# Performance work log

Hardware: AMD Instinct MI355X
Metric: run time of the kernel (lower is better)

Reference implementation:

```python
import math
import jax, jax.numpy as jnp
import numpy as np

H = 16       # num_heads
DH = 128     # head_dim (q/k)
DV = 128     # value_head_dim
CHUNK = 1024 # chunk_size
BASE = 10000.0  # rope base


def _rope(q, k, start_index):
    # q, k: (B, L, H, Dh); rotate pair-split halves (x1|x2 layout, not interleaved)
    B, L, h, d = q.shape
    half = d // 2
    freqs = jnp.exp(jnp.arange(half, dtype=jnp.float32) * (-math.log(BASE) / half))
    t = (jnp.arange(L, dtype=jnp.float32) + start_index)[:, None] * freqs[None, :]  # (L, half)
    cos = jnp.cos(t)[None, :, None, :].astype(q.dtype)
    sin = jnp.sin(t)[None, :, None, :].astype(q.dtype)

    def rot(x):
        x1, x2 = jnp.split(x, 2, axis=-1)
        return jnp.concatenate([x1 * cos - x2 * sin, x2 * cos + x1 * sin], axis=-1)

    return rot(q), rot(k)


def setup_inputs() -> dict:
    key = jax.random.key(0)
    kq, kk, kv = jax.random.split(key, 3)
    B, L = 2, 4096
    q = jax.random.normal(kq, (B, L, H, DH), dtype=jnp.float32)
    k = jax.random.normal(kk, (B, L, H, DH), dtype=jnp.float32)
    v = jax.random.normal(kv, (B, L, H, DV), dtype=jnp.float32)
    return {"q": q, "k": k, "v": v, "start_index": 0}


def reference(q, k, v, start_index):
    # Training path of ChunkedSelfAttention: L > chunk_size, no cache/attn_mask.
    B, L, h, d = q.shape
    q, k = _rope(q, k, start_index)
    nc = L // CHUNK
    # (B, nc, H, C, D) -- chunks never attend across boundaries
    qc = q.reshape(B, nc, CHUNK, h, d).transpose(0, 1, 3, 2, 4)
    kc = k.reshape(B, nc, CHUNK, h, d).transpose(0, 1, 3, 2, 4)
    vc = v.reshape(B, nc, CHUNK, h, DV).transpose(0, 1, 3, 2, 4)
    scores = jnp.einsum('bnhqd,bnhkd->bnhqk', qc, kc) / math.sqrt(d)
    i = jnp.arange(CHUNK)
    causal = i[:, None] >= i[None, :]  # (C, C)
    scores = jnp.where(causal, scores, -jnp.inf)
    attn = jax.nn.softmax(scores.astype(jnp.float32), axis=-1).astype(q.dtype)
    out = jnp.einsum('bnhqk,bnhkv->bnhqv', attn, vc)
    out = out.transpose(0, 1, 3, 2, 4).reshape(B, L, h * DV)
    return out
```

## Files before the change

kernel.cpp:

```cpp
#include <hip/hip_runtime.h>
#include <math.h>

#define NB 2
#define SEQL 4096
#define NH 16
#define HD 128
#define HDV 128
#define CHK 1024
#define NC 4
#define BQ 128
#define BK 64
#define KSTR 136
#define VSTR 72
#define OUTW 2048
#define NEGB (-1e30f)
#define L2B64 0.20762050593045702f

typedef _Float16 f16x8 __attribute__((ext_vector_type(8)));
typedef float f32x4 __attribute__((ext_vector_type(4)));
typedef unsigned short u16x8 __attribute__((ext_vector_type(8)));

static __device__ __forceinline__ unsigned short f2h(float f) {
  return __builtin_bit_cast(unsigned short, (_Float16)f);
}
static __device__ __forceinline__ f16x8 ld8(const unsigned short* p) {
  return __builtin_bit_cast(f16x8, *(const u16x8*)p);
}
static __device__ __forceinline__ void fast_sincos(float t, float* sn, float* cs) {
  const float INV2PI = 0.15915494309189535f;
  const float TWOPI  = 6.283185307179586f;
  float rev = t * INV2PI;
  rev -= floorf(rev);
  float ang = rev * TWOPI;
  *sn = __sinf(ang);
  *cs = __cosf(ang);
}
static __device__ __forceinline__ void gload16(const void* g, void* l) {
  __builtin_amdgcn_global_load_lds(
      (const __attribute__((address_space(1))) unsigned int*)g,
      (__attribute__((address_space(3))) unsigned int*)l, 16, 0, 0);
}

#define DPPF(x, ctrl)                                                            \
  __builtin_bit_cast(float, __builtin_amdgcn_update_dpp(                         \
      __builtin_bit_cast(int, x), __builtin_bit_cast(int, x), ctrl, 0xF, 0xF, true))
static __device__ __forceinline__ float dpp16_max(float x) {
  x = fmaxf(x, DPPF(x, 0xB1));
  x = fmaxf(x, DPPF(x, 0x4E));
  x = fmaxf(x, DPPF(x, 0x141));
  x = fmaxf(x, DPPF(x, 0x140));
  return x;
}
static __device__ __forceinline__ float dpp16_sum(float x) {
  x += DPPF(x, 0xB1);
  x += DPPF(x, 0x4E);
  x += DPPF(x, 0x141);
  x += DPPF(x, 0x140);
  return x;
}

__global__ __launch_bounds__(256) void megalodon_prep(
    const float* __restrict__ k, const float* __restrict__ v,
    unsigned short* __restrict__ kr, unsigned short* __restrict__ vt,
    const int* __restrict__ startp) {
  const int tid = threadIdx.x;
  const int blk = blockIdx.x;
  if (blk < 4096) {
    const int s0 = startp[0];
    const int gr = blk * 32 + (tid >> 3);
    const int c0 = (tid & 7) * 8;
    const int h  = gr & 15;
    const int bl = gr >> 4;
    const int l  = bl & (SEQL - 1);
    const int b  = bl >> 12;
    const int n  = l >> 10;
    const int rc = l & (CHK - 1);
    const int jt = rc >> 6;
    const int r  = rc & 63;
    const float* kp = k + (size_t)gr * HD;
    float xa[8], xb[8];
    *(f32x4*)&xa[0] = *(const f32x4*)(kp + c0);
    *(f32x4*)&xa[4] = *(const f32x4*)(kp + c0 + 4);
    *(f32x4*)&xb[0] = *(const f32x4*)(kp + c0 + 64);
    *(f32x4*)&xb[4] = *(const f32x4*)(kp + c0 + 68);
    u16x8 lo, hi;
#pragma unroll
    for (int jj = 0; jj < 8; ++jj) {
      const int dd = c0 + jj;
      float freq = exp2f(-L2B64 * (float)dd);
      float t = (float)(l + s0) * freq;
      float sn, cs;
      fast_sincos(t, &sn, &cs);
      lo[jj] = f2h(xa[jj] * cs - xb[jj] * sn);
      hi[jj] = f2h(xb[jj] * cs + xa[jj] * sn);
    }
    unsigned short* dst = kr + ((size_t)(((b * NH + h) * NC + n) * 16 + jt)) * 8192;
    const int sw = (r & 7) << 3;
    *(u16x8*)&dst[(r * 128 + c0) ^ sw]      = lo;
    *(u16x8*)&dst[(r * 128 + c0 + 64) ^ sw] = hi;
  } else {
    const int tv = blk - 4096;
    const int jt = tv & 15;
    const int n  = (tv >> 4) & 3;
    const int h  = (tv >> 6) & 15;
    const int b  = tv >> 10;
    unsigned short* dst = vt + ((size_t)(((b * NH + h) * NC + n) * 16 + jt)) * 8192;
#pragma unroll
    for (int it = 0; it < 4; ++it) {
      const int idx = tid + it * 256;
      const int vc = idx & 127;
      const int kg = idx >> 7;
      const int lbase = n * CHK + jt * 64 + kg * 8;
      u16x8 vv;
#pragma unroll
      for (int i = 0; i < 8; ++i)
        vv[i] = f2h(v[((size_t)(b * SEQL + lbase + i) * NH + h) * HDV + vc]);
      *(u16x8*)&dst[(vc * 64 + kg * 8) ^ ((vc & 7) << 3)] = vv;
    }
  }
}

__global__ __launch_bounds__(256) void megalodon_attn2(
    const float* __restrict__ q,
    const unsigned short* __restrict__ kr,
    const unsigned short* __restrict__ vt,
    float* __restrict__ out,
    const int* __restrict__ startp) {

  __shared__ __align__(16) unsigned short smem[24576];

  const int tid  = threadIdx.x;
  const int lane = tid & 63;
  const int wv   = tid >> 6;
  const int ln15 = lane & 15;
  const int quad = lane >> 4;

  const int bid = blockIdx.x;
  const int qt = 7 - (bid >> 7);
  const int h  = bid & 15;
  const int n  = (bid >> 4) & 3;
  const int b  = (bid >> 6) & 1;

  const int s0 = startp[0];
  const float scale = 0.08838834764831845f;
  const int l0 = n * CHK + qt * BQ;

  f16x8 qf[2][4];
#pragma unroll
  for (int rt = 0; rt < 2; ++rt) {
    const int l = l0 + wv * 32 + rt * 16 + ln15;
    const float* qp = q + ((size_t)(b * SEQL + l) * NH + h) * HD;
#pragma unroll
    for (int kf2 = 0; kf2 < 2; ++kf2) {
      const int c0 = kf2 * 32 + quad * 8;
      float xa[8], xb[8];
      *(f32x4*)&xa[0] = *(const f32x4*)(qp + c0);
      *(f32x4*)&xa[4] = *(const f32x4*)(qp + c0 + 4);
      *(f32x4*)&xb[0] = *(const f32x4*)(qp + c0 + 64);
      *(f32x4*)&xb[4] = *(const f32x4*)(qp + c0 + 68);
      f16x8 lo, hi;
#pragma unroll
      for (int j = 0; j < 8; ++j) {
        const int dd = c0 + j;
        float x1 = xa[j];
        float x2 = xb[j];
        float freq = exp2f(-L2B64 * (float)dd);
        float t = (float)(l + s0) * freq;
        float sn, cs;
        fast_sincos(t, &sn, &cs);
        lo[j] = (_Float16)((x1 * cs - x2 * sn) * scale);
        hi[j] = (_Float16)((x2 * cs + x1 * sn) * scale);
      }
      qf[rt][kf2]     = lo;
      qf[rt][kf2 + 2] = hi;
    }
  }

  f32x4 oacc[2][8];
  float m_run[2][4], l_run[2][4];
#pragma unroll
  for (int rt = 0; rt < 2; ++rt) {
#pragma unroll
    for (int vq = 0; vq < 8; ++vq) { f32x4 z = {0.f, 0.f, 0.f, 0.f}; oacc[rt][vq] = z; }
#pragma unroll
    for (int rg = 0; rg < 4; ++rg) { m_run[rt][rg] = NEGB; l_run[rt][rg] = 0.f; }
  }

  const size_t tb0 = (size_t)(((b * NH + h) * NC + n)) * 16;
  const int ksw = (ln15 & 7) << 3;

  auto stageK = [&](int t) {
    const char* ks = (const char*)kr + ((tb0 + t) << 14) + wv * 4096 + lane * 16;
    char* kd = ((char*)smem) + ((t & 1) << 14) + wv * 4096;
#pragma unroll
    for (int i = 0; i < 4; ++i) gload16(ks + i * 1024, kd + i * 1024);
  };
  auto stageV = [&](int t) {
    const char* vs = (const char*)vt + ((tb0 + t) << 14) + wv * 4096 + lane * 16;
    char* vd = ((char*)smem) + 32768 + wv * 4096;
#pragma unroll
    for (int i = 0; i < 4; ++i) gload16(vs + i * 1024, vd + i * 1024);
  };

  const int ntiles = 2 * qt + 2;
  stageK(0);
  stageV(0);
  for (int j = 0; j < ntiles; ++j) {
    const int cur = j & 1;
    if (j + 1 < ntiles) {
      stageK(j + 1);
      asm volatile("s_waitcnt vmcnt(8)" ::: "memory");
    } else {
      asm volatile("s_waitcnt vmcnt(4)" ::: "memory");
    }
    __builtin_amdgcn_s_barrier();

    const unsigned short* sK  = smem + cur * 8192;
    const unsigned short* sVT = smem + 16384;
    const bool act = (j * BK <= qt * BQ + wv * 32 + 31);

    f32x4 sacc[2][4];
    if (act) {
#pragma unroll
      for (int rt = 0; rt < 2; ++rt)
#pragma unroll
        for (int ct = 0; ct < 4; ++ct) { f32x4 z = {0.f, 0.f, 0.f, 0.f}; sacc[rt][ct] = z; }
      __builtin_amdgcn_s_setprio(1);
#pragma unroll
      for (int ct = 0; ct < 4; ++ct) {
#pragma unroll
        for (int kf = 0; kf < 4; ++kf) {
          f16x8 kb = ld8(&sK[(((ct * 16 + ln15) * 128) + kf * 32 + quad * 8) ^ ksw]);
          sacc[0][ct] = __builtin_amdgcn_mfma_f32_16x16x32_f16(qf[0][kf], kb, sacc[0][ct], 0, 0, 0);
          sacc[1][ct] = __builtin_amdgcn_mfma_f32_16x16x32_f16(qf[1][kf], kb, sacc[1][ct], 0, 0, 0);
        }
      }
      __builtin_amdgcn_s_setprio(0);
    }

    __builtin_amdgcn_s_barrier();
    unsigned short* sP = smem + cur * 8192;

    if (act) {
      const int colb = j * BK + ln15;
      float alpha[2][4];
#pragma unroll
      for (int rt = 0; rt < 2; ++rt) {
        const int rowq = qt * BQ + wv * 32 + rt * 16 + quad * 4;
#pragma unroll
        for (int rg = 0; rg < 4; ++rg) {
          const int row = rowq + rg;
          float mx = NEGB;
#pragma unroll
          for (int ct = 0; ct < 4; ++ct) {
            float sv = sacc[rt][ct][rg];
            sv = (colb + ct * 16 <= row) ? sv : NEGB;
            sacc[rt][ct][rg] = sv;
            mx = fmaxf(mx, sv);
          }
          mx = dpp16_max(mx);
          float mo = m_run[rt][rg];
          float mn = fmaxf(mo, mx);
          m_run[rt][rg] = mn;
          float al = __expf(mo - mn);
          alpha[rt][rg] = al;
          float rs = 0.f;
          const int prow = rt * 16 + quad * 4 + rg;
          const int psw = ((quad * 4 + rg) & 7) << 3;
#pragma unroll
          for (int ct = 0; ct < 4; ++ct) {
            float p = __expf(sacc[rt][ct][rg] - mn);
            rs += p;
            sP[wv * 2048 + ((prow * 64 + ct * 16 + ln15) ^ psw)] = f2h(p);
          }
          rs = dpp16_sum(rs);
          l_run[rt][rg] = l_run[rt][rg] * al + rs;
        }
      }
#pragma unroll
      for (int rt = 0; rt < 2; ++rt)
#pragma unroll
        for (int vq = 0; vq < 8; ++vq)
#pragma unroll
          for (int rg = 0; rg < 4; ++rg) oacc[rt][vq][rg] *= alpha[rt][rg];
    }

    if (j + 1 < ntiles)
      asm volatile("s_waitcnt vmcnt(4)" ::: "memory");
    else
      asm volatile("s_waitcnt vmcnt(0)" ::: "memory");
    __builtin_amdgcn_s_barrier();

    if (act) {
      asm volatile("s_waitcnt lgkmcnt(0)" ::: "memory");
      __builtin_amdgcn_s_setprio(1);
#pragma unroll
      for (int kf = 0; kf < 2; ++kf) {
        f16x8 pa0 = ld8(&sP[wv * 2048 + ((ln15 * 64 + kf * 32 + quad * 8) ^ ksw)]);
        f16x8 pa1 = ld8(&sP[wv * 2048 + (((16 + ln15) * 64 + kf * 32 + quad * 8) ^ ksw)]);
#pragma unroll
        for (int vq = 0; vq < 8; ++vq) {
          f16x8 vb = ld8(&sVT[(((vq * 16 + ln15) * 64) + kf * 32 + quad * 8) ^ ksw]);
          oacc[0][vq] = __builtin_amdgcn_mfma_f32_16x16x32_f16(pa0, vb, oacc[0][vq], 0, 0, 0);
          oacc[1][vq] = __builtin_amdgcn_mfma_f32_16x16x32_f16(pa1, vb, oacc[1][vq], 0, 0, 0);
        }
      }
      __builtin_amdgcn_s_setprio(0);
    }

    __builtin_amdgcn_s_barrier();
    if (j + 1 < ntiles) stageV(j + 1);
  }

#pragma unroll
  for (int rt = 0; rt < 2; ++rt) {
#pragma unroll
    for (int rg = 0; rg < 4; ++rg) {
      const int l = l0 + wv * 32 + rt * 16 + quad * 4 + rg;
      const float lr = l_run[rt][rg];
      const float inv = (lr > 0.f) ? (1.0f / lr) : 0.f;
      float* op = out + (size_t)(b * SEQL + l) * OUTW + h * HDV + ln15;
#pragma unroll
      for (int vq = 0; vq < 8; ++vq)
        op[vq * 16] = oacc[rt][vq][rg] * inv;
    }
  }
}

__global__ __launch_bounds__(256) void megalodon_attn_k(
    const float* __restrict__ q,
    const float* __restrict__ k,
    const float* __restrict__ v,
    float* __restrict__ out,
    const int* __restrict__ startp) {

  __shared__ __align__(16) unsigned short smem[27136];
  unsigned short* sK  = smem;
  unsigned short* sVT = smem + 8704;
  unsigned short* sP  = smem + 17920;

  const int tid  = threadIdx.x;
  const int lane = tid & 63;
  const int wv   = tid >> 6;
  const int ln15 = lane & 15;
  const int quad = lane >> 4;

  const int bid = blockIdx.x;
  const int qt  = bid & 7;
  const int h   = (bid >> 3) & 15;
  const int n   = (bid >> 7) & 3;
  const int b   = bid >> 9;

  const int s0 = startp[0];
  const float scale = 0.08838834764831845f;
  const int l0 = n * CHK + qt * BQ;

  f16x8 qf[2][4];
#pragma unroll
  for (int rt = 0; rt < 2; ++rt) {
    const int l = l0 + wv * 32 + rt * 16 + ln15;
    const float* qp = q + ((size_t)(b * SEQL + l) * NH + h) * HD;
#pragma unroll
    for (int kf2 = 0; kf2 < 2; ++kf2) {
      const int c0 = kf2 * 32 + quad * 8;
      float xa[8], xb[8];
      *(f32x4*)&xa[0] = *(const f32x4*)(qp + c0);
      *(f32x4*)&xa[4] = *(const f32x4*)(qp + c0 + 4);
      *(f32x4*)&xb[0] = *(const f32x4*)(qp + c0 + 64);
      *(f32x4*)&xb[4] = *(const f32x4*)(qp + c0 + 68);
      f16x8 lo, hi;
#pragma unroll
      for (int j = 0; j < 8; ++j) {
        const int dd = c0 + j;
        float x1 = xa[j];
        float x2 = xb[j];
        float freq = exp2f(-L2B64 * (float)dd);
        float t = (float)(l + s0) * freq;
        float sn, cs;
        fast_sincos(t, &sn, &cs);
        lo[j] = (_Float16)((x1 * cs - x2 * sn) * scale);
        hi[j] = (_Float16)((x2 * cs + x1 * sn) * scale);
      }
      qf[rt][kf2]     = lo;
      qf[rt][kf2 + 2] = hi;
    }
  }

  f32x4 oacc[2][8];
  float m_run[2][4], l_run[2][4];
#pragma unroll
  for (int rt = 0; rt < 2; ++rt) {
#pragma unroll
    for (int vt = 0; vt < 8; ++vt) { f32x4 z = {0.f, 0.f, 0.f, 0.f}; oacc[rt][vt] = z; }
#pragma unroll
    for (int rg = 0; rg < 4; ++rg) { m_run[rt][rg] = NEGB; l_run[rt][rg] = 0.f; }
  }

  const float kfreq = exp2f(-L2B64 * (float)(tid & 63));

  const int ntiles = 2 * qt + 2;
  for (int j = 0; j < ntiles; ++j) {
    __syncthreads();
    const int kl0 = n * CHK + j * BK;

    for (int idx = tid; idx < BK * 64; idx += 256) {
      int r = idx >> 6, dd = idx & 63;
      int l = kl0 + r;
      const float* kp = k + ((size_t)(b * SEQL + l) * NH + h) * HD;
      float x1 = kp[dd];
      float x2 = kp[dd + 64];
      float t = (float)(l + s0) * kfreq;
      float sn, cs;
      fast_sincos(t, &sn, &cs);
      sK[r * KSTR + dd]      = f2h(x1 * cs - x2 * sn);
      sK[r * KSTR + dd + 64] = f2h(x2 * cs + x1 * sn);
    }
    for (int idx = tid; idx < HDV * (BK / 8); idx += 256) {
      int vc = idx & 127;
      int sk = idx >> 7;
      u16x8 vv;
#pragma unroll
      for (int i = 0; i < 8; ++i)
        vv[i] = f2h(v[((size_t)(b * SEQL + kl0 + sk * 8 + i) * NH + h) * HDV + vc]);
      *(u16x8*)&sVT[vc * VSTR + sk * 8] = vv;
    }
    __syncthreads();

    if (j * BK <= qt * BQ + wv * 32 + 31) {
      f32x4 sacc[2][4];
#pragma unroll
      for (int rt = 0; rt < 2; ++rt)
#pragma unroll
        for (int ct = 0; ct < 4; ++ct) { f32x4 z = {0.f, 0.f, 0.f, 0.f}; sacc[rt][ct] = z; }
#pragma unroll
      for (int ct = 0; ct < 4; ++ct) {
#pragma unroll
        for (int kf = 0; kf < 4; ++kf) {
          f16x8 kb = ld8(&sK[(ct * 16 + ln15) * KSTR + kf * 32 + quad * 8]);
          sacc[0][ct] = __builtin_amdgcn_mfma_f32_16x16x32_f16(qf[0][kf], kb, sacc[0][ct], 0, 0, 0);
          sacc[1][ct] = __builtin_amdgcn_mfma_f32_16x16x32_f16(qf[1][kf], kb, sacc[1][ct], 0, 0, 0);
        }
      }

      const int colb = j * BK + ln15;
      float alpha[2][4];
#pragma unroll
      for (int rt = 0; rt < 2; ++rt) {
        const int rowq = qt * BQ + wv * 32 + rt * 16 + quad * 4;
#pragma unroll
        for (int rg = 0; rg < 4; ++rg) {
          const int row = rowq + rg;
          float mx = NEGB;
#pragma unroll
          for (int ct = 0; ct < 4; ++ct) {
            float sv = sacc[rt][ct][rg];
            sv = (colb + ct * 16 <= row) ? sv : NEGB;
            sacc[rt][ct][rg] = sv;
            mx = fmaxf(mx, sv);
          }
          mx = fmaxf(mx, __shfl_xor(mx, 1));
          mx = fmaxf(mx, __shfl_xor(mx, 2));
          mx = fmaxf(mx, __shfl_xor(mx, 4));
          mx = fmaxf(mx, __shfl_xor(mx, 8));
          float mo = m_run[rt][rg];
          float mn = fmaxf(mo, mx);
          m_run[rt][rg] = mn;
          float al = __expf(mo - mn);
          alpha[rt][rg] = al;
          float rs = 0.f;
#pragma unroll
          for (int ct = 0; ct < 4; ++ct) {
            float p = __expf(sacc[rt][ct][rg] - mn);
            rs += p;
            sP[wv * (32 * VSTR) + (rt * 16 + quad * 4 + rg) * VSTR + ct * 16 + ln15] = f2h(p);
          }
          rs += __shfl_xor(rs, 1);
          rs += __shfl_xor(rs, 2);
          rs += __shfl_xor(rs, 4);
          rs += __shfl_xor(rs, 8);
          l_run[rt][rg] = l_run[rt][rg] * al + rs;
        }
      }
#pragma unroll
      for (int rt = 0; rt < 2; ++rt)
#pragma unroll
        for (int vt = 0; vt < 8; ++vt)
#pragma unroll
          for (int rg = 0; rg < 4; ++rg) oacc[rt][vt][rg] *= alpha[rt][rg];

      asm volatile("s_waitcnt lgkmcnt(0)" ::: "memory");

#pragma unroll
      for (int kf = 0; kf < 2; ++kf) {
        f16x8 pa0 = ld8(&sP[wv * (32 * VSTR) + (ln15)*VSTR + kf * 32 + quad * 8]);
        f16x8 pa1 = ld8(&sP[wv * (32 * VSTR) + (16 + ln15) * VSTR + kf * 32 + quad * 8]);
#pragma unroll
        for (int vt = 0; vt < 8; ++vt) {
          f16x8 vb = ld8(&sVT[(vt * 16 + ln15) * VSTR + kf * 32 + quad * 8]);
          oacc[0][vt] = __builtin_amdgcn_mfma_f32_16x16x32_f16(pa0, vb, oacc[0][vt], 0, 0, 0);
          oacc[1][vt] = __builtin_amdgcn_mfma_f32_16x16x32_f16(pa1, vb, oacc[1][vt], 0, 0, 0);
        }
      }
    }
  }

#pragma unroll
  for (int rt = 0; rt < 2; ++rt) {
#pragma unroll
    for (int rg = 0; rg < 4; ++rg) {
      const int l = l0 + wv * 32 + rt * 16 + quad * 4 + rg;
      const float lr = l_run[rt][rg];
      const float inv = (lr > 0.f) ? (1.0f / lr) : 0.f;
      float* op = out + (size_t)(b * SEQL + l) * OUTW + h * HDV + ln15;
#pragma unroll
      for (int vt = 0; vt < 8; ++vt)
        op[vt * 16] = oacc[rt][vt][rg] * inv;
    }
  }
}

extern "C" void kernel_launch(void* const* d_in, const int* in_sizes, int n_in,
                              void* d_out, int out_size, void* d_ws, size_t ws_size,
                              hipStream_t stream) {
  const float* q = (const float*)d_in[0];
  const float* k = (const float*)d_in[1];
  const float* v = (const float*)d_in[2];
  const int* start = (const int*)d_in[3];
  (void)in_sizes; (void)n_in; (void)out_size;

  const size_t NEED = 64ull * 1024 * 1024;
  if (d_ws != nullptr && ws_size >= NEED) {
    unsigned short* kr = (unsigned short*)d_ws;
    unsigned short* vt = kr + 16777216;
    megalodon_prep<<<6144, 256, 0, stream>>>(k, v, kr, vt, start);
    megalodon_attn2<<<NB * 4 * NH * 8, 256, 0, stream>>>(q, kr, vt, (float*)d_out, start);
  } else {
    megalodon_attn_k<<<NB * 4 * NH * 8, 256, 0, stream>>>(q, k, v, (float*)d_out, start);
  }
}
```

Measured before the change: 334.8 us.

## Use 8 waves of 16 rows each and double-buffer K and V together

The attention kernel moves from 4 waves with 32 query rows each to 8 waves with 16 rows each. This halves the per-wave registers for Q fragments, accumulators and softmax state, and launch bounds now request more resident waves. K and V tiles are loaded together into double-buffered shared memory, which removes a barrier and the separate V stage at the end of each iteration. Shared memory grows to 64KB, which can cap blocks per CU, and each K/V fragment read from LDS now feeds only one MFMA instead of two, so LDS traffic per FLOP doubles.

```diff
diff --git a/kernel.cpp b/kernel.cpp
--- a/kernel.cpp
+++ b/kernel.cpp
@@ -120,14 +120,14 @@
   }
 }
 
-__global__ __launch_bounds__(256) void megalodon_attn2(
+__global__ __launch_bounds__(512, 4) void megalodon_attn2(
     const float* __restrict__ q,
     const unsigned short* __restrict__ kr,
     const unsigned short* __restrict__ vt,
     float* __restrict__ out,
     const int* __restrict__ startp) {
 
-  __shared__ __align__(16) unsigned short smem[24576];
+  __shared__ __align__(16) unsigned short smem[32768];
 
   const int tid  = threadIdx.x;
   const int lane = tid & 63;
@@ -144,11 +144,11 @@
   const int s0 = startp[0];
   const float scale = 0.08838834764831845f;
   const int l0 = n * CHK + qt * BQ;
-
-  f16x8 qf[2][4];
-#pragma unroll
-  for (int rt = 0; rt < 2; ++rt) {
-    const int l = l0 + wv * 32 + rt * 16 + ln15;
+  const int rowbase = qt * BQ + wv * 16;
+
+  f16x8 qf[4];
+  {
+    const int l = l0 + wv * 16 + ln15;
     const float* qp = q + ((size_t)(b * SEQL + l) * NH + h) * HD;
 #pragma unroll
     for (int kf2 = 0; kf2 < 2; ++kf2) {
@@ -171,159 +171,127 @@
         lo[j] = (_Float16)((x1 * cs - x2 * sn) * scale);
         hi[j] = (_Float16)((x2 * cs + x1 * sn) * scale);
       }
-      qf[rt][kf2]     = lo;
-      qf[rt][kf2 + 2] = hi;
-    }
-  }
-
-  f32x4 oacc[2][8];
-  float m_run[2][4], l_run[2][4];
-#pragma unroll
-  for (int rt = 0; rt < 2; ++rt) {
-#pragma unroll
-    for (int vq = 0; vq < 8; ++vq) { f32x4 z = {0.f, 0.f, 0.f, 0.f}; oacc[rt][vq] = z; }
-#pragma unroll
-    for (int rg = 0; rg < 4; ++rg) { m_run[rt][rg] = NEGB; l_run[rt][rg] = 0.f; }
-  }
+      qf[kf2]     = lo;
+      qf[kf2 + 2] = hi;
+    }
+  }
+
+  f32x4 oacc[8];
+  float m_run[4], l_run[4];
+#pragma unroll
+  for (int vq = 0; vq < 8; ++vq) { f32x4 z = {0.f, 0.f, 0.f, 0.f}; oacc[vq] = z; }
+#pragma unroll
+  for (int rg = 0; rg < 4; ++rg) { m_run[rg] = NEGB; l_run[rg] = 0.f; }
 
   const size_t tb0 = (size_t)(((b * NH + h) * NC + n)) * 16;
   const int ksw = (ln15 & 7) << 3;
 
-  auto stageK = [&](int t) {
-    const char* ks = (const char*)kr + ((tb0 + t) << 14) + wv * 4096 + lane * 16;
-    char* kd = ((char*)smem) + ((t & 1) << 14) + wv * 4096;
-#pragma unroll
-    for (int i = 0; i < 4; ++i) gload16(ks + i * 1024, kd + i * 1024);
+  auto stage = [&](int t) {
+    const char* ks = (const char*)kr + ((tb0 + t) << 14) + wv * 2048 + lane * 16;
+    const char* vs = (const char*)vt + ((tb0 + t) << 14) + wv * 2048 + lane * 16;
+    char* kd = ((char*)smem) + ((t & 1) << 14) + wv * 2048;
+    char* vd = ((char*)smem) + 32768 + ((t & 1) << 14) + wv * 2048;
+    gload16(ks, kd);
+    gload16(ks + 1024, kd + 1024);
+    gload16(vs, vd);
+    gload16(vs + 1024, vd + 1024);
   };
-  auto stageV = [&](int t) {
-    const char* vs = (const char*)vt + ((tb0 + t) << 14) + wv * 4096 + lane * 16;
-    char* vd = ((char*)smem) + 32768 + wv * 4096;
-#pragma unroll
-    for (int i = 0; i < 4; ++i) gload16(vs + i * 1024, vd + i * 1024);
-  };
 
   const int ntiles = 2 * qt + 2;
-  stageK(0);
-  stageV(0);
+  stage(0);
   for (int j = 0; j < ntiles; ++j) {
     const int cur = j & 1;
     if (j + 1 < ntiles) {
-      stageK(j + 1);
-      asm volatile("s_waitcnt vmcnt(8)" ::: "memory");
+      stage(j + 1);
+      asm volatile("s_waitcnt vmcnt(4)" ::: "memory");
     } else {
-      asm volatile("s_waitcnt vmcnt(4)" ::: "memory");
+      asm volatile("s_waitcnt vmcnt(0)" ::: "memory");
     }
     __builtin_amdgcn_s_barrier();
 
     const unsigned short* sK  = smem + cur * 8192;
-    const unsigned short* sVT = smem + 16384;
-    const bool act = (j * BK <= qt * BQ + wv * 32 + 31);
-
-    f32x4 sacc[2][4];
+    const unsigned short* sVT = smem + 16384 + cur * 8192;
+    const bool act = (j * BK <= rowbase + 15);
+
+    f32x4 sacc[4];
     if (act) {
 #pragma unroll
-      for (int rt = 0; rt < 2; ++rt)
-#pragma unroll
-        for (int ct = 0; ct < 4; ++ct) { f32x4 z = {0.f, 0.f, 0.f, 0.f}; sacc[rt][ct] = z; }
+      for (int ct = 0; ct < 4; ++ct) { f32x4 z = {0.f, 0.f, 0.f, 0.f}; sacc[ct] = z; }
       __builtin_amdgcn_s_setprio(1);
 #pragma unroll
       for (int ct = 0; ct < 4; ++ct) {
 #pragma unroll
         for (int kf = 0; kf < 4; ++kf) {
           f16x8 kb = ld8(&sK[(((ct * 16 + ln15) * 128) + kf * 32 + quad * 8) ^ ksw]);
-          sacc[0][ct] = __builtin_amdgcn_mfma_f32_16x16x32_f16(qf[0][kf], kb, sacc[0][ct], 0, 0, 0);
-          sacc[1][ct] = __builtin_amdgcn_mfma_f32_16x16x32_f16(qf[1][kf], kb, sacc[1][ct], 0, 0, 0);
+          sacc[ct] = __builtin_amdgcn_mfma_f32_16x16x32_f16(qf[kf], kb, sacc[ct], 0, 0, 0);
         }
       }
       __builtin_amdgcn_s_setprio(0);
     }
 
     __builtin_amdgcn_s_barrier();
-    unsigned short* sP = smem + cur * 8192;
+    unsigned short* sP = smem + cur * 8192 + wv * 1024;
 
     if (act) {
       const int colb = j * BK + ln15;
-      float alpha[2][4];
-#pragma unroll
-      for (int rt = 0; rt < 2; ++rt) {
-        const int rowq = qt * BQ + wv * 32 + rt * 16 + quad * 4;
-#pragma unroll
-        for (int rg = 0; rg < 4; ++rg) {
-          const int row = rowq + rg;
-          float mx = NEGB;
-#pragma unroll
-          for (int ct = 0; ct < 4; ++ct) {
-            float sv = sacc[rt][ct][rg];
-            sv = (colb + ct * 16 <= row) ? sv : NEGB;
-            sacc[rt][ct][rg] = sv;
-            mx = fmaxf(mx, sv);
-          }
-          mx = dpp16_max(mx);
-          float mo = m_run[rt][rg];
-          float mn = fmaxf(mo, mx);
-          m_run[rt][rg] = mn;
-          float al = __expf(mo - mn);
-          alpha[rt][rg] = al;
-          float rs = 0.f;
-          const int prow = rt * 16 + quad * 4 + rg;
-          const int psw = ((quad * 4 + rg) & 7) << 3;
-#pragma unroll
-          for (int ct = 0; ct < 4; ++ct) {
-            float p = __expf(sacc[rt][ct][rg] - mn);
-            rs += p;
-            sP[wv * 2048 + ((prow * 64 + ct * 16 + ln15) ^ psw)] = f2h(p);
-          }
-          rs = dpp16_sum(rs);
-          l_run[rt][rg] = l_run[rt][rg] * al + rs;
-        }
-      }
-#pragma unroll
-      for (int rt = 0; rt < 2; ++rt)
-#pragma unroll
-        for (int vq = 0; vq < 8; ++vq)
-#pragma unroll
-          for (int rg = 0; rg < 4; ++rg) oacc[rt][vq][rg] *= alpha[rt][rg];
-    }
-
-    if (j + 1 < ntiles)
-      asm volatile("s_waitcnt vmcnt(4)" ::: "memory");
-    else
-      asm volatile("s_waitcnt vmcnt(0)" ::: "memory");
-    __builtin_amdgcn_s_barrier();
-
-    if (act) {
+#pragma unroll
+      for (int rg = 0; rg < 4; ++rg) {
+        const int row = rowbase + quad * 4 + rg;
+        float mx = NEGB;
+#pragma unroll
+        for (int ct = 0; ct < 4; ++ct) {
+          float sv = sacc[ct][rg];
+          sv = (colb + ct * 16 <= row) ? sv : NEGB;
+          sacc[ct][rg] = sv;
+          mx = fmaxf(mx, sv);
+        }
+        mx = dpp16_max(mx);
+        float mo = m_run[rg];
+        float mn = fmaxf(mo, mx);
+        m_run[rg] = mn;
+        float al = __expf(mo - mn);
+        float rs = 0.f;
+        const int pr = quad * 4 + rg;
+        const int psw = (pr & 7) << 3;
+#pragma unroll
+        for (int ct = 0; ct < 4; ++ct) {
+          float p = __expf(sacc[ct][rg] - mn);
+          rs += p;
+          sP[(pr * 64 + ct * 16 + ln15) ^ psw] = f2h(p);
+        }
+        rs = dpp16_sum(rs);
+        l_run[rg] = l_run[rg] * al + rs;
+#pragma unroll
+        for (int vq = 0; vq < 8; ++vq) oacc[vq][rg] *= al;
+      }
+
       asm volatile("s_waitcnt lgkmcnt(0)" ::: "memory");
+
       __builtin_amdgcn_s_setprio(1);
 #pragma unroll
       for (int kf = 0; kf < 2; ++kf) {
-        f16x8 pa0 = ld8(&sP[wv * 2048 + ((ln15 * 64 + kf * 32 + quad * 8) ^ ksw)]);
-        f16x8 pa1 = ld8(&sP[wv * 2048 + (((16 + ln15) * 64 + kf * 32 + quad * 8) ^ ksw)]);
+        f16x8 pa = ld8(&sP[(ln15 * 64 + kf * 32 + quad * 8) ^ ksw]);
 #pragma unroll
         for (int vq = 0; vq < 8; ++vq) {
           f16x8 vb = ld8(&sVT[(((vq * 16 + ln15) * 64) + kf * 32 + quad * 8) ^ ksw]);
-          oacc[0][vq] = __builtin_amdgcn_mfma_f32_16x16x32_f16(pa0, vb, oacc[0][vq], 0, 0, 0);
-          oacc[1][vq] = __builtin_amdgcn_mfma_f32_16x16x32_f16(pa1, vb, oacc[1][vq], 0, 0, 0);
+          oacc[vq] = __builtin_amdgcn_mfma_f32_16x16x32_f16(pa, vb, oacc[vq], 0, 0, 0);
         }
       }
       __builtin_amdgcn_s_setprio(0);
     }
 
     __builtin_amdgcn_s_barrier();
-    if (j + 1 < ntiles) stageV(j + 1);
-  }
-
-#pragma unroll
-  for (int rt = 0; rt < 2; ++rt) {
-#pragma unroll
-    for (int rg = 0; rg < 4; ++rg) {
-      const int l = l0 + wv * 32 + rt * 16 + quad * 4 + rg;
-      const float lr = l_run[rt][rg];
-      const float inv = (lr > 0.f) ? (1.0f / lr) : 0.f;
-      float* op = out + (size_t)(b * SEQL + l) * OUTW + h * HDV + ln15;
-#pragma unroll
-      for (int vq = 0; vq < 8; ++vq)
-        op[vq * 16] = oacc[rt][vq][rg] * inv;
-    }
+  }
+
+#pragma unroll
+  for (int rg = 0; rg < 4; ++rg) {
+    const int l = l0 + wv * 16 + quad * 4 + rg;
+    const float lr = l_run[rg];
+    const float inv = (lr > 0.f) ? (1.0f / lr) : 0.f;
+    float* op = out + (size_t)(b * SEQL + l) * OUTW + h * HDV + ln15;
+#pragma unroll
+    for (int vq = 0; vq < 8; ++vq)
+      op[vq * 16] = oacc[vq][rg] * inv;
   }
 }
 
@@ -533,7 +501,7 @@
     unsigned short* kr = (unsigned short*)d_ws;
     unsigned short* vt = kr + 16777216;
     megalodon_prep<<<6144, 256, 0, stream>>>(k, v, kr, vt, start);
-    megalodon_attn2<<<NB * 4 * NH * 8, 256, 0, stream>>>(q, kr, vt, (float*)d_out, start);
+    megalodon_attn2<<<NB * 4 * NH * 8, 512, 0, stream>>>(q, kr, vt, (float*)d_out, start);
   } else {
     megalodon_attn_k<<<NB * 4 * NH * 8, 256, 0, stream>>>(q, k, v, (float*)d_out, start);
   }
```

Measured after the change: 341.2 us. Within noise of the previous version (+1.9%).

## Double query tile to 256 rows with 512-thread blocks and double-buffered K/V

Applied to the files above, without the earlier changes.

The attention kernel now processes 256 query rows per block using 8 waves (512 threads), which halves the grid and doubles how often each staged K/V tile is reused. K and V are now both double-buffered, with P given its own LDS region, so each key tile needs only one wait plus one barrier instead of three barriers. The cost is lower parallelism (512 blocks) and coarser causal load imbalance across blocks. The next stage is issued right after the barrier following a full vmcnt(0) wait, so there is less overlap between loads and compute.

```diff
diff --git a/kernel.cpp b/kernel.cpp
--- a/kernel.cpp
+++ b/kernel.cpp
@@ -8,7 +8,7 @@
 #define HDV 128
 #define CHK 1024
 #define NC 4
-#define BQ 128
+#define BQ 256
 #define BK 64
 #define KSTR 136
 #define VSTR 72
@@ -120,14 +120,14 @@
   }
 }
 
-__global__ __launch_bounds__(256) void megalodon_attn2(
+__global__ __launch_bounds__(512) void megalodon_attn2(
     const float* __restrict__ q,
     const unsigned short* __restrict__ kr,
     const unsigned short* __restrict__ vt,
     float* __restrict__ out,
     const int* __restrict__ startp) {
 
-  __shared__ __align__(16) unsigned short smem[24576];
+  __shared__ __align__(16) unsigned short smem[49152];
 
   const int tid  = threadIdx.x;
   const int lane = tid & 63;
@@ -136,7 +136,7 @@
   const int quad = lane >> 4;
 
   const int bid = blockIdx.x;
-  const int qt = 7 - (bid >> 7);
+  const int qt = 3 - ((bid >> 7) & 3);
   const int h  = bid & 15;
   const int n  = (bid >> 4) & 3;
   const int b  = (bid >> 6) & 1;
@@ -144,6 +144,7 @@
   const int s0 = startp[0];
   const float scale = 0.08838834764831845f;
   const int l0 = n * CHK + qt * BQ;
+  const int rowbase = qt * BQ + wv * 32;
 
   f16x8 qf[2][4];
 #pragma unroll
@@ -189,38 +190,32 @@
   const size_t tb0 = (size_t)(((b * NH + h) * NC + n)) * 16;
   const int ksw = (ln15 & 7) << 3;
 
-  auto stageK = [&](int t) {
-    const char* ks = (const char*)kr + ((tb0 + t) << 14) + wv * 4096 + lane * 16;
-    char* kd = ((char*)smem) + ((t & 1) << 14) + wv * 4096;
-#pragma unroll
-    for (int i = 0; i < 4; ++i) gload16(ks + i * 1024, kd + i * 1024);
+  auto stage = [&](int t) {
+    const char* ks = (const char*)kr + ((tb0 + t) << 14) + wv * 2048 + lane * 16;
+    const char* vs = (const char*)vt + ((tb0 + t) << 14) + wv * 2048 + lane * 16;
+    char* kd = ((char*)smem) + ((t & 1) << 14) + wv * 2048;
+    char* vd = ((char*)smem) + 32768 + ((t & 1) << 14) + wv * 2048;
+    gload16(ks, kd);
+    gload16(ks + 1024, kd + 1024);
+    gload16(vs, vd);
+    gload16(vs + 1024, vd + 1024);
   };
-  auto stageV = [&](int t) {
-    const char* vs = (const char*)vt + ((tb0 + t) << 14) + wv * 4096 + lane * 16;
-    char* vd = ((char*)smem) + 32768 + wv * 4096;
-#pragma unroll
-    for (int i = 0; i < 4; ++i) gload16(vs + i * 1024, vd + i * 1024);
-  };
-
-  const int ntiles = 2 * qt + 2;
-  stageK(0);
-  stageV(0);
+
+  const int ntiles = 4 * qt + 4;
+  stage(0);
   for (int j = 0; j < ntiles; ++j) {
     const int cur = j & 1;
-    if (j + 1 < ntiles) {
-      stageK(j + 1);
-      asm volatile("s_waitcnt vmcnt(8)" ::: "memory");
-    } else {
-      asm volatile("s_waitcnt vmcnt(4)" ::: "memory");
-    }
+    asm volatile("s_waitcnt vmcnt(0)" ::: "memory");
     __builtin_amdgcn_s_barrier();
+    if (j + 1 < ntiles) stage(j + 1);
 
     const unsigned short* sK  = smem + cur * 8192;
-    const unsigned short* sVT = smem + 16384;
-    const bool act = (j * BK <= qt * BQ + wv * 32 + 31);
-
-    f32x4 sacc[2][4];
+    const unsigned short* sVT = smem + 16384 + cur * 8192;
+    unsigned short* sP = smem + 32768 + wv * 2048;
+    const bool act = (j * BK <= rowbase + 31);
+
     if (act) {
+      f32x4 sacc[2][4];
 #pragma unroll
       for (int rt = 0; rt < 2; ++rt)
 #pragma unroll
@@ -236,17 +231,12 @@
         }
       }
       __builtin_amdgcn_s_setprio(0);
-    }
-
-    __builtin_amdgcn_s_barrier();
-    unsigned short* sP = smem + cur * 8192;
-
-    if (act) {
+
       const int colb = j * BK + ln15;
       float alpha[2][4];
 #pragma unroll
       for (int rt = 0; rt < 2; ++rt) {
-        const int rowq = qt * BQ + wv * 32 + rt * 16 + quad * 4;
+        const int rowq = rowbase + rt * 16 + quad * 4;
 #pragma unroll
         for (int rg = 0; rg < 4; ++rg) {
           const int row = rowq + rg;
@@ -271,7 +261,7 @@
           for (int ct = 0; ct < 4; ++ct) {
             float p = __expf(sacc[rt][ct][rg] - mn);
             rs += p;
-            sP[wv * 2048 + ((prow * 64 + ct * 16 + ln15) ^ psw)] = f2h(p);
+            sP[(prow * 64 + ct * 16 + ln15) ^ psw] = f2h(p);
           }
           rs = dpp16_sum(rs);
           l_run[rt][rg] = l_run[rt][rg] * al + rs;
@@ -283,21 +273,14 @@
         for (int vq = 0; vq < 8; ++vq)
 #pragma unroll
           for (int rg = 0; rg < 4; ++rg) oacc[rt][vq][rg] *= alpha[rt][rg];
-    }
-
-    if (j + 1 < ntiles)
-      asm volatile("s_waitcnt vmcnt(4)" ::: "memory");
-    else
-      asm volatile("s_waitcnt vmcnt(0)" ::: "memory");
-    __builtin_amdgcn_s_barrier();
-
-    if (act) {
+
       asm volatile("s_waitcnt lgkmcnt(0)" ::: "memory");
+
       __builtin_amdgcn_s_setprio(1);
 #pragma unroll
       for (int kf = 0; kf < 2; ++kf) {
-        f16x8 pa0 = ld8(&sP[wv * 2048 + ((ln15 * 64 + kf * 32 + quad * 8) ^ ksw)]);
-        f16x8 pa1 = ld8(&sP[wv * 2048 + (((16 + ln15) * 64 + kf * 32 + quad * 8) ^ ksw)]);
+        f16x8 pa0 = ld8(&sP[(ln15 * 64 + kf * 32 + quad * 8) ^ ksw]);
+        f16x8 pa1 = ld8(&sP[((16 + ln15) * 64 + kf * 32 + quad * 8) ^ ksw]);
 #pragma unroll
         for (int vq = 0; vq < 8; ++vq) {
           f16x8 vb = ld8(&sVT[(((vq * 16 + ln15) * 64) + kf * 32 + quad * 8) ^ ksw]);
@@ -307,9 +290,6 @@
       }
       __builtin_amdgcn_s_setprio(0);
     }
-
-    __builtin_amdgcn_s_barrier();
-    if (j + 1 < ntiles) stageV(j + 1);
   }
 
 #pragma unroll
@@ -353,7 +333,7 @@
 
   const int s0 = startp[0];
   const float scale = 0.08838834764831845f;
-  const int l0 = n * CHK + qt * BQ;
+  const int l0 = n * CHK + qt * 128;
 
   f16x8 qf[2][4];
 #pragma unroll
@@ -426,7 +406,7 @@
     }
     __syncthreads();
 
-    if (j * BK <= qt * BQ + wv * 32 + 31) {
+    if (j * BK <= qt * 128 + wv * 32 + 31) {
       f32x4 sacc[2][4];
 #pragma unroll
       for (int rt = 0; rt < 2; ++rt)
@@ -446,7 +426,7 @@
       float alpha[2][4];
 #pragma unroll
       for (int rt = 0; rt < 2; ++rt) {
-        const int rowq = qt * BQ + wv * 32 + rt * 16 + quad * 4;
+        const int rowq = qt * 128 + wv * 32 + rt * 16 + quad * 4;
 #pragma unroll
         for (int rg = 0; rg < 4; ++rg) {
           const int row = rowq + rg;
@@ -533,7 +513,7 @@
     unsigned short* kr = (unsigned short*)d_ws;
     unsigned short* vt = kr + 16777216;
     megalodon_prep<<<6144, 256, 0, stream>>>(k, v, kr, vt, start);
-    megalodon_attn2<<<NB * 4 * NH * 8, 256, 0, stream>>>(q, kr, vt, (float*)d_out, start);
+    megalodon_attn2<<<512, 512, 0, stream>>>(q, kr, vt, (float*)d_out, start);
   } else {
     megalodon_attn_k<<<NB * 4 * NH * 8, 256, 0, stream>>>(q, k, v, (float*)d_out, start);
   }
```

Result: faster. 285.7 us (-14.7%).
